# Performance work log

Measured on AMD Instinct MI355X. Metric: run time of the kernel, lower is better.

## Reference

```python
import jax, jax.numpy as jnp
import numpy as np

B, D, N, L, H, M = 8, 128, 307, 12, 8, 4
DK = D // H  # 16
APT = 10
EPS = 1e-5


def _conv1x1(x, W, b):
    # 1x1 Conv2d over channel dim: x [B,C,N,L], W [O,C], b [O]
    return jnp.einsum('bcnl,oc->bonl', x, W) + b[None, :, None, None]


def _ln12(t):
    # custom LayerNorm: normalize over dims (1,2), no affine
    m = t.mean(axis=(1, 2), keepdims=True)
    v = t.var(axis=(1, 2), keepdims=True)
    return (t - m) / jnp.sqrt(v + EPS)


def _forward(x, Wq, bq, Wv, bv, Wc, bc, Wx, bx, Wg1, bg1, Wg2, bg2, Wg3, bg3,
             mem_bank, mem_imp, A1, a1b, A2, a2b, weight, bias, nv1, nv2, sws):
    # --- multi-scale adjacency from learned node vectors ---
    base = jax.nn.relu(nv1 @ nv2)                       # [N,N]
    s1 = jax.nn.softmax(base, axis=-1)
    s2 = jax.nn.softmax(s1 @ s1, axis=-1)
    s3 = jax.nn.softmax(s2 @ s1, axis=-1)
    sw = jax.nn.softmax(sws)                            # [3]

    # --- q/v projections (Conv = 1x1 conv + ReLU; dropout off in eval) ---
    q = jax.nn.relu(_conv1x1(x, Wq, bq))
    v = jax.nn.relu(_conv1x1(x, Wv, bv))
    q5 = q.reshape(B, H, DK, N, L).transpose(0, 1, 4, 3, 2)  # bhlnk
    v5 = v.reshape(B, H, DK, N, L).transpose(0, 1, 4, 3, 2)  # bhlnk

    # --- adaptive memory retrieval ---
    avg = x.mean(axis=(2, 3))                           # [B,D]
    mem_attn = jax.nn.softmax(jax.nn.relu(avg @ A1 + a1b) @ A2 + a2b, axis=-1)  # [B,M]
    mem_w = jax.nn.softmax(mem_imp * mem_attn, axis=-1)
    sel = jnp.einsum('bm,mhlnk->bhlnk', mem_w, mem_bank)

    # --- attention against selected memory ---
    logits = jnp.einsum('bhlnk,bhlmk->bhlnm', q5, sel) / np.sqrt(DK).astype(np.float32)
    attn = jax.nn.softmax(logits, axis=-1)
    aqkv = jnp.einsum('bhlnm,bhlmk->bhlnk', attn, v5)

    # --- 3-scale graph diffusion (einsum linear in adj, so combine first) ---
    adj = sw[0] * s1 + sw[1] * s2 + sw[2] * s3          # [N,N]
    agraph = jnp.einsum('nm,bhlnk->bhlmk', adj, v5)

    y = aqkv + agraph
    y = y.transpose(0, 1, 4, 3, 2).reshape(B, D, N, L)
    y = y + _conv1x1(y, Wx, bx)                         # cross_dim_proj residual
    y = jax.nn.relu(_conv1x1(y, Wc, bc))                # concat Conv
    y = y * weight + bias + y                           # N=307 not in [170,358,5]

    # --- EnhancedEncoder wrapper ---
    z = _ln12(y + x)
    res = z
    g = _conv1x1(z, Wg1, bg1) * jax.nn.sigmoid(_conv1x1(z, Wg2, bg2))
    g = _conv1x1(g, Wg3, bg3)
    z = g + res
    z = z * weight + bias + z
    z = _ln12(z)
    return z


def setup_inputs() -> dict:
    key = jax.random.key(0)
    ks = iter(jax.random.split(key, 40))
    def rn(shape, s=0.05):
        return jax.random.normal(next(ks), shape, dtype=jnp.float32) * s
    inp = {'x': jax.random.normal(next(ks), (B, D, N, L), dtype=jnp.float32)}
    for nm in ['Wq', 'Wv', 'Wc', 'Wx', 'Wg1', 'Wg2', 'Wg3']:
        inp[nm] = rn((D, D))
        inp['b' + nm[1:]] = jnp.zeros((D,), jnp.float32)
    inp['mem_bank'] = rn((M, H, L, N, DK), 0.1)
    inp['mem_imp'] = jnp.ones((M,), jnp.float32)
    inp['A1'] = rn((D, D // 2)); inp['a1b'] = jnp.zeros((D // 2,), jnp.float32)
    inp['A2'] = rn((D // 2, M)); inp['a2b'] = jnp.zeros((M,), jnp.float32)
    inp['weight'] = jnp.ones((D, N, L), jnp.float32) + rn((D, N, L), 0.01)
    inp['bias'] = rn((D, N, L), 0.01)
    inp['nv1'] = rn((N, APT), 1.0)
    inp['nv2'] = rn((APT, N), 1.0)
    inp['sws'] = jnp.ones((3,), jnp.float32)
    return inp


def reference(x, Wq, bq, Wv, bv, Wc, bc, Wx, bx, Wg1, bg1, Wg2, bg2, Wg3, bg3,
              mem_bank, mem_imp, A1, a1b, A2, a2b, weight, bias, nv1, nv2, sws):
    return _forward(x, Wq, bq, Wv, bv, Wc, bc, Wx, bx, Wg1, bg1, Wg2, bg2, Wg3, bg3,
                    mem_bank, mem_imp, A1, a1b, A2, a2b, weight, bias, nv1, nv2, sws)
```

## Files before the change

### kernel.cpp

```cpp
#include <hip/hip_runtime.h>

namespace {

constexpr int NN   = 307;
constexpr int LNUM = 12;
constexpr int SP   = NN * LNUM;
constexpr int DCH  = 128;
constexpr int HH   = 8;
constexpr int DK   = 16;
constexpr int BB   = 8;
constexpr int SZB  = DCH * SP;
constexpr int SZ   = BB * SZB;
constexpr int ADJN = NN * NN;
constexpr int DN   = DCH * NN;
constexpr int LN_RCH = 58;
constexpr int MST  = HH * LNUM * NN * DK;

typedef __attribute__((ext_vector_type(8))) short short8_t;
typedef __attribute__((ext_vector_type(4))) float f32x4;

__device__ inline unsigned short f2bf(float f) {
  unsigned int u = __builtin_bit_cast(unsigned int, f);
  unsigned int r = (u + 0x7FFFu + ((u >> 16) & 1u)) >> 16;
  return (unsigned short)r;
}
__device__ inline float bf2f(unsigned short h) {
  unsigned int u = ((unsigned int)h) << 16;
  return __builtin_bit_cast(float, u);
}

__device__ __host__ inline int posm(int m) {
  int q = (m & 15) >> 2, sub = (m >> 4) & 1, i = m & 3;
  return (m & ~31) + 8 * q + 4 * sub + i;
}


__global__ __launch_bounds__(256) void k_cvtW(
    const float* __restrict__ W0, const float* __restrict__ W1,
    const float* __restrict__ W2, const float* __restrict__ W3,
    const float* __restrict__ W4, const float* __restrict__ W5,
    const float* __restrict__ W6, unsigned int* __restrict__ Wb) {
  const float* srcs[7] = {W0, W1, W2, W3, W4, W5, W6};
  int idx = blockIdx.x * 256 + threadIdx.x;
  int w = idx >> 13, off = idx & 8191;
  const float* s = srcs[w];
  float v0 = s[off * 2], v1 = s[off * 2 + 1];
  unsigned int pk;
  asm("v_cvt_pk_bf16_f32 %0, %1, %2" : "=v"(pk) : "v"(v0), "v"(v1));
  Wb[idx] = pk;
}

__global__ __launch_bounds__(320) void k_s1(
    const float* __restrict__ nv1, const float* __restrict__ nv2,
    float* __restrict__ out) {
  __shared__ float red[512];
  __shared__ float rowA[10];
  const int i = blockIdx.x, j = threadIdx.x;
  if (j < 10) rowA[j] = nv1[i * 10 + j];
  __syncthreads();
  float val = 0.f;
  if (j < NN) {
#pragma unroll
    for (int k = 0; k < 10; ++k) val += rowA[k] * nv2[k * NN + j];
    val = fmaxf(val, 0.f);
  }
  red[j] = (j < NN) ? val : -3.4e38f;
  if (j < 192) red[j + 320] = -3.4e38f;
  __syncthreads();
  for (int s = 256; s >= 1; s >>= 1) {
    if (j < s) red[j] = fmaxf(red[j], red[j + s]);
    __syncthreads();
  }
  float mx = red[0];
  __syncthreads();
  float e = (j < NN) ? __expf(val - mx) : 0.f;
  red[j] = e;
  if (j < 192) red[j + 320] = 0.f;
  __syncthreads();
  for (int s = 256; s >= 1; s >>= 1) {
    if (j < s) red[j] += red[j + s];
    __syncthreads();
  }
  if (j < NN) out[i * NN + j] = e / red[0];
}

__global__ __launch_bounds__(320) void k_smm(
    const float* __restrict__ Sa, const float* __restrict__ Sb,
    float* __restrict__ out) {
  __shared__ float red[512];
  __shared__ float rowA[320];
  const int i = blockIdx.x, j = threadIdx.x;
  if (j < NN) rowA[j] = Sa[i * NN + j];
  __syncthreads();
  float val = 0.f;
  if (j < NN) {
    for (int k = 0; k < NN; ++k) val += rowA[k] * Sb[k * NN + j];
  }
  red[j] = (j < NN) ? val : -3.4e38f;
  if (j < 192) red[j + 320] = -3.4e38f;
  __syncthreads();
  for (int s = 256; s >= 1; s >>= 1) {
    if (j < s) red[j] = fmaxf(red[j], red[j + s]);
    __syncthreads();
  }
  float mx = red[0];
  __syncthreads();
  float e = (j < NN) ? __expf(val - mx) : 0.f;
  red[j] = e;
  if (j < 192) red[j + 320] = 0.f;
  __syncthreads();
  for (int s = 256; s >= 1; s >>= 1) {
    if (j < s) red[j] += red[j + s];
    __syncthreads();
  }
  if (j < NN) out[i * NN + j] = e / red[0];
}

__global__ __launch_bounds__(256) void k_adjT(
    const float* __restrict__ s1, const float* __restrict__ s2,
    const float* __restrict__ s3, const float* __restrict__ sws,
    unsigned int* __restrict__ adjTw) {
  int idx = blockIdx.x * 256 + threadIdx.x;
  if (idx >= 320 * 160) return;
  int n = idx / 160, wp = idx - n * 160;
  int pos0 = 2 * wp;
  int bq = pos0 & 31;
  int g = bq >> 3, sub = (bq >> 2) & 1, i = bq & 3;
  int m0 = (pos0 & ~31) + sub * 16 + 4 * g + i;
  float w0 = sws[0], w1 = sws[1], w2 = sws[2];
  float mm = fmaxf(w0, fmaxf(w1, w2));
  float e0 = __expf(w0 - mm), e1 = __expf(w1 - mm), e2 = __expf(w2 - mm);
  float inv = 1.f / (e0 + e1 + e2);
  e0 *= inv; e1 *= inv; e2 *= inv;
  float v0 = 0.f, v1 = 0.f;
  if (n < NN) {
    if (m0 < NN)     v0 = e0 * s1[m0 * NN + n] + e1 * s2[m0 * NN + n] + e2 * s3[m0 * NN + n];
    if (m0 + 1 < NN) v1 = e0 * s1[(m0 + 1) * NN + n] + e1 * s2[(m0 + 1) * NN + n] + e2 * s3[(m0 + 1) * NN + n];
  }
  adjTw[n * 160 + wp] = (unsigned int)f2bf(v0) | ((unsigned int)f2bf(v1) << 16);
}

__global__ __launch_bounds__(256) void k_avg(
    const float* __restrict__ x, float* __restrict__ avg) {
  const int row = blockIdx.x * 4 + (threadIdx.x >> 6);
  const int lane = threadIdx.x & 63;
  const float* p = x + (size_t)row * SP;
  float s = 0.f;
  for (int i = lane; i < SP / 4; i += 64) {
    float4 v = *(const float4*)(p + i * 4);
    s += v.x + v.y + v.z + v.w;
  }
  s += __shfl_xor(s, 1);  s += __shfl_xor(s, 2);  s += __shfl_xor(s, 4);
  s += __shfl_xor(s, 8);  s += __shfl_xor(s, 16); s += __shfl_xor(s, 32);
  if (lane == 0) avg[row] = s * (1.f / SP);
}

__global__ __launch_bounds__(128) void k_memw2(
    const float* __restrict__ avgg, const float* __restrict__ A1,
    const float* __restrict__ a1b, const float* __restrict__ A2,
    const float* __restrict__ a2b, const float* __restrict__ mimp,
    float* __restrict__ memw) {
  const int b = blockIdx.x, t = threadIdx.x;
  __shared__ float avg[128];
  __shared__ float hbuf[64];
  __shared__ float lg[4];
  avg[t] = avgg[b * 128 + t];
  __syncthreads();
  if (t < 64) {
    float a = a1b[t];
    for (int d = 0; d < 128; ++d) a += avg[d] * A1[d * 64 + t];
    hbuf[t] = fmaxf(a, 0.f);
  }
  __syncthreads();
  if (t < 4) {
    float a = a2b[t];
    for (int j = 0; j < 64; ++j) a += hbuf[j] * A2[j * 4 + t];
    lg[t] = a;
  }
  __syncthreads();
  if (t == 0) {
    float mx = fmaxf(fmaxf(lg[0], lg[1]), fmaxf(lg[2], lg[3]));
    float e[4]; float se = 0.f;
    for (int m = 0; m < 4; ++m) { e[m] = __expf(lg[m] - mx); se += e[m]; }
    float w[4]; float mx2 = -3.4e38f;
    for (int m = 0; m < 4; ++m) { w[m] = mimp[m] * (e[m] / se); mx2 = fmaxf(mx2, w[m]); }
    float se2 = 0.f;
    for (int m = 0; m < 4; ++m) { e[m] = __expf(w[m] - mx2); se2 += e[m]; }
    for (int m = 0; m < 4; ++m) memw[b * 4 + m] = e[m] / se2;
  }
}

__global__ __launch_bounds__(256) void k_convqv(
    const unsigned short* __restrict__ Wqb, const unsigned short* __restrict__ Wvb,
    const float* __restrict__ X, const float* __restrict__ bq,
    const float* __restrict__ bv, unsigned short* __restrict__ qb,
    unsigned short* __restrict__ vb) {
  __shared__ unsigned short Xs[64 * 128];
  __shared__ unsigned short Ws[128 * 128];
  const int sBase = blockIdx.x * 64;
  const int b = blockIdx.z;
  const int t = threadIdx.x;

  {
    const int u = t & 63, cp = t >> 6;
    const int s = sBase + u;
    const bool in = s < SP;
#pragma unroll
    for (int it = 0; it < 16; ++it) {
      int c0 = it * 8 + cp * 2;
      float v0 = 0.f, v1 = 0.f;
      if (in) {
        v0 = X[(size_t)(b * DCH + c0) * SP + s];
        v1 = X[(size_t)(b * DCH + c0 + 1) * SP + s];
      }
      unsigned int pk;
      asm("v_cvt_pk_bf16_f32 %0, %1, %2" : "=v"(pk) : "v"(v0), "v"(v1));
      *(unsigned int*)((char*)Xs + u * 256 + ((2 * c0) ^ ((u & 7) << 4))) = pk;
    }
  }
  const int o = t >> 1, half = t & 1;
  {
    const unsigned short* src = Wqb + o * 128 + half * 64;
#pragma unroll
    for (int j = 0; j < 8; ++j) {
      short8_t v = *(const short8_t*)(src + j * 8);
      *(short8_t*)((char*)Ws + o * 256 + ((half * 128 + j * 16) ^ ((o & 7) << 4))) = v;
    }
  }
  __syncthreads();

  const int wave = t >> 6, lane = t & 63;
  const int r = lane & 15, g = lane >> 4;
  const int swz = (r & 7) << 4;

  short8_t xa[4];
#pragma unroll
  for (int kk = 0; kk < 4; ++kk)
    xa[kk] = *(const short8_t*)((const char*)Xs + (wave * 16 + r) * 256 + ((kk * 64 + g * 16) ^ swz));

  const f32x4 zf = {0.f, 0.f, 0.f, 0.f};
  const int s0 = sBase + wave * 16 + 4 * g;
  const bool act = s0 < SP;

  {
    f32x4 acc[8];
#pragma unroll
    for (int ot = 0; ot < 8; ++ot) acc[ot] = zf;
#pragma unroll
    for (int ot = 0; ot < 8; ++ot) {
#pragma unroll
      for (int kk = 0; kk < 4; ++kk) {
        short8_t wb = *(const short8_t*)((const char*)Ws + (ot * 16 + r) * 256 + ((kk * 64 + g * 16) ^ swz));
        acc[ot] = __builtin_amdgcn_mfma_f32_16x16x32_bf16(xa[kk], wb, acc[ot], 0, 0, 0);
      }
    }
    if (act) {
#pragma unroll
      for (int ot = 0; ot < 8; ++ot) {
        float bvv = bq[ot * 16 + r];
#pragma unroll
        for (int i = 0; i < 4; ++i) {
          int s = s0 + i, n = s / 12, l2 = s - n * 12;
          qb[((b * 8 + ot) * 12 + l2) * 5120 + n * 16 + r] = f2bf(fmaxf(acc[ot][i] + bvv, 0.f));
        }
      }
    }
  }
  __syncthreads();
  {
    const unsigned short* src = Wvb + o * 128 + half * 64;
#pragma unroll
    for (int j = 0; j < 8; ++j) {
      short8_t v = *(const short8_t*)(src + j * 8);
      *(short8_t*)((char*)Ws + o * 256 + ((half * 128 + j * 16) ^ ((o & 7) << 4))) = v;
    }
  }
  __syncthreads();
  {
    f32x4 acc[8];
#pragma unroll
    for (int ot = 0; ot < 8; ++ot) acc[ot] = zf;
#pragma unroll
    for (int ot = 0; ot < 8; ++ot) {
#pragma unroll
      for (int kk = 0; kk < 4; ++kk) {
        short8_t wb = *(const short8_t*)((const char*)Ws + (ot * 16 + r) * 256 + ((kk * 64 + g * 16) ^ swz));
        acc[ot] = __builtin_amdgcn_mfma_f32_16x16x32_bf16(xa[kk], wb, acc[ot], 0, 0, 0);
      }
    }
    if (act) {
#pragma unroll
      for (int ot = 0; ot < 8; ++ot) {
        float bvv = bv[ot * 16 + r];
#pragma unroll
        for (int i = 0; i < 4; ++i) {
          int s = s0 + i, n = s / 12, l2 = s - n * 12;
          vb[((b * 8 + ot) * 12 + l2) * 5120 + r * 320 + posm(n)] = f2bf(fmaxf(acc[ot][i] + bvv, 0.f));
        }
      }
    }
  }
}

__global__ __launch_bounds__(256) void k_conv12(
    const unsigned short* __restrict__ Wxb, const unsigned short* __restrict__ Wcb,
    const unsigned short* __restrict__ yRp, const float* __restrict__ bx,
    const float* __restrict__ bc, const float* __restrict__ aw,
    const float* __restrict__ ab, const float* __restrict__ axf,
    unsigned short* __restrict__ outR) {
  __shared__ unsigned short Xs[64 * 128];
  __shared__ unsigned short Ws[128 * 128];
  const int sBase = blockIdx.x * 64;
  const int b = blockIdx.z;
  const int t = threadIdx.x;

  {
    const int sl = t >> 2, q = t & 3;
    const int s = sBase + sl;
    const short8_t z8 = {0, 0, 0, 0, 0, 0, 0, 0};
    const unsigned short* row = yRp + (((size_t)b * SP + s) << 7);
#pragma unroll
    for (int j = 0; j < 4; ++j) {
      int cb = 16 * (4 * j + q);
      short8_t v = (s < SP) ? *(const short8_t*)((const char*)row + cb) : z8;
      *(short8_t*)((char*)Xs + sl * 256 + (cb ^ ((sl & 7) << 4))) = v;
    }
  }
  const int o = t >> 1, half = t & 1;
  {
    const unsigned short* src = Wxb + o * 128 + half * 64;
#pragma unroll
    for (int j = 0; j < 8; ++j) {
      short8_t v = *(const short8_t*)(src + j * 8);
      *(short8_t*)((char*)Ws + o * 256 + ((half * 128 + j * 16) ^ ((o & 7) << 4))) = v;
    }
  }
  __syncthreads();

  const int wave = t >> 6, lane = t & 63;
  const int r = lane & 15, g = lane >> 4;
  const int swz = (r & 7) << 4;
  const int s0 = sBase + wave * 16 + 4 * g;
  const bool act = s0 < SP;

  short8_t xa[4];
#pragma unroll
  for (int kk = 0; kk < 4; ++kk)
    xa[kk] = *(const short8_t*)((const char*)Xs + (wave * 16 + r) * 256 + ((kk * 64 + g * 16) ^ swz));

  const f32x4 zf = {0.f, 0.f, 0.f, 0.f};
  f32x4 acc[8];
#pragma unroll
  for (int ot = 0; ot < 8; ++ot) acc[ot] = zf;
#pragma unroll
  for (int ot = 0; ot < 8; ++ot) {
#pragma unroll
    for (int kk = 0; kk < 4; ++kk) {
      short8_t wb = *(const short8_t*)((const char*)Ws + (ot * 16 + r) * 256 + ((kk * 64 + g * 16) ^ swz));
      acc[ot] = __builtin_amdgcn_mfma_f32_16x16x32_bf16(xa[kk], wb, acc[ot], 0, 0, 0);
    }
  }

  unsigned short tpk[8][4];
  if (act) {
#pragma unroll
    for (int ot = 0; ot < 8; ++ot) {
      int oo = ot * 16 + r;
      float bvv = bx[oo];
#pragma unroll
      for (int i = 0; i < 4; ++i) {
        int u = wave * 16 + 4 * g + i;
        float y = bf2f(*(const unsigned short*)((const char*)Xs + u * 256 + ((2 * oo) ^ ((u & 7) << 4))));
        tpk[ot][i] = f2bf(acc[ot][i] + bvv + y);
      }
    }
  }
  __syncthreads();

  if (act) {
#pragma unroll
    for (int ot = 0; ot < 8; ++ot) {
      int oo = ot * 16 + r;
#pragma unroll
      for (int i = 0; i < 4; ++i) {
        int u = wave * 16 + 4 * g + i;
        *(unsigned short*)((char*)Xs + u * 256 + ((2 * oo) ^ ((u & 7) << 4))) = tpk[ot][i];
      }
    }
  }
  {
    const unsigned short* src = Wcb + o * 128 + half * 64;
#pragma unroll
    for (int j = 0; j < 8; ++j) {
      short8_t v = *(const short8_t*)(src + j * 8);
      *(short8_t*)((char*)Ws + o * 256 + ((half * 128 + j * 16) ^ ((o & 7) << 4))) = v;
    }
  }
  __syncthreads();

#pragma unroll
  for (int kk = 0; kk < 4; ++kk)
    xa[kk] = *(const short8_t*)((const char*)Xs + (wave * 16 + r) * 256 + ((kk * 64 + g * 16) ^ swz));
#pragma unroll
  for (int ot = 0; ot < 8; ++ot) acc[ot] = zf;
#pragma unroll
  for (int ot = 0; ot < 8; ++ot) {
#pragma unroll
    for (int kk = 0; kk < 4; ++kk) {
      short8_t wb = *(const short8_t*)((const char*)Ws + (ot * 16 + r) * 256 + ((kk * 64 + g * 16) ^ swz));
      acc[ot] = __builtin_amdgcn_mfma_f32_16x16x32_bf16(xa[kk], wb, acc[ot], 0, 0, 0);
    }
  }

  if (!act) return;
#pragma unroll
  for (int ot = 0; ot < 8; ++ot) {
    int oo = ot * 16 + r;
    float bvv = bc[oo];
    float4 w4 = *(const float4*)(aw + oo * SP + s0);
    float4 b4 = *(const float4*)(ab + oo * SP + s0);
    float4 x4 = *(const float4*)(axf + (size_t)(b * DCH + oo) * SP + s0);
#pragma unroll
    for (int i = 0; i < 4; ++i) {
      float rr = fmaxf(acc[ot][i] + bvv, 0.f);
      float val = rr * ((&w4.x)[i] + 1.f) + (&b4.x)[i] + (&x4.x)[i];
      outR[(((size_t)b * SP + s0 + i) << 7) + oo] = f2bf(val);
    }
  }
}

__global__ __launch_bounds__(256) void k_conv345(
    const unsigned short* __restrict__ Wb1, const unsigned short* __restrict__ Wb2,
    const unsigned short* __restrict__ Wb3, const unsigned short* __restrict__ Zr,
    const float* __restrict__ b1, const float* __restrict__ b2,
    const float* __restrict__ b3, const float* __restrict__ meanp,
    const float* __restrict__ rstdp, const float* __restrict__ aw,
    const float* __restrict__ ab, unsigned short* __restrict__ outR) {
  __shared__ unsigned short Xs[64 * 128];
  __shared__ unsigned short Ws[128 * 128];
  const int sBase = blockIdx.x * 64;
  const int b = blockIdx.z;
  const int t = threadIdx.x;

  {
    const int sl = t >> 2, q = t & 3;
    const int s = sBase + sl;
    float m = 0.f, rr = 0.f;
    if (s < SP) { int l = s % 12; m = meanp[b * 12 + l]; rr = rstdp[b * 12 + l]; }
    const short8_t z8 = {0, 0, 0, 0, 0, 0, 0, 0};
    const unsigned short* row = Zr + (((size_t)b * SP + s) << 7);
#pragma unroll
    for (int j = 0; j < 4; ++j) {
      int cb = 16 * (4 * j + q);
      short8_t v = (s < SP) ? *(const short8_t*)((const char*)row + cb) : z8;
      union { unsigned int w[4]; short8_t s8; } u;
#pragma unroll
      for (int k2 = 0; k2 < 4; ++k2) {
        float f0 = (bf2f((unsigned short)v[2 * k2]) - m) * rr;
        float f1 = (bf2f((unsigned short)v[2 * k2 + 1]) - m) * rr;
        asm("v_cvt_pk_bf16_f32 %0, %1, %2" : "=v"(u.w[k2]) : "v"(f0), "v"(f1));
      }
      *(short8_t*)((char*)Xs + sl * 256 + (cb ^ ((sl & 7) << 4))) = u.s8;
    }
  }
  const int o = t >> 1, half = t & 1;
  {
    const unsigned short* src = Wb1 + o * 128 + half * 64;
#pragma unroll
    for (int j = 0; j < 8; ++j) {
      short8_t v = *(const short8_t*)(src + j * 8);
      *(short8_t*)((char*)Ws + o * 256 + ((half * 128 + j * 16) ^ ((o & 7) << 4))) = v;
    }
  }
  __syncthreads();

  const int wave = t >> 6, lane = t & 63;
  const int r = lane & 15, g = lane >> 4;
  const int swz = (r & 7) << 4;
  const int s0 = sBase + wave * 16 + 4 * g;
  const bool act = s0 < SP;

  short8_t xa[4];
#pragma unroll
  for (int kk = 0; kk < 4; ++kk)
    xa[kk] = *(const short8_t*)((const char*)Xs + (wave * 16 + r) * 256 + ((kk * 64 + g * 16) ^ swz));

  const f32x4 zf = {0.f, 0.f, 0.f, 0.f};
  f32x4 acc1[8], acc2[8];
#pragma unroll
  for (int ot = 0; ot < 8; ++ot) { acc1[ot] = zf; acc2[ot] = zf; }
#pragma unroll
  for (int ot = 0; ot < 8; ++ot) {
#pragma unroll
    for (int kk = 0; kk < 4; ++kk) {
      short8_t wb = *(const short8_t*)((const char*)Ws + (ot * 16 + r) * 256 + ((kk * 64 + g * 16) ^ swz));
      acc1[ot] = __builtin_amdgcn_mfma_f32_16x16x32_bf16(xa[kk], wb, acc1[ot], 0, 0, 0);
    }
  }
  __syncthreads();
  {
    const unsigned short* src = Wb2 + o * 128 + half * 64;
#pragma unroll
    for (int j = 0; j < 8; ++j) {
      short8_t v = *(const short8_t*)(src + j * 8);
      *(short8_t*)((char*)Ws + o * 256 + ((half * 128 + j * 16) ^ ((o & 7) << 4))) = v;
    }
  }
  __syncthreads();
#pragma unroll
  for (int ot = 0; ot < 8; ++ot) {
#pragma unroll
    for (int kk = 0; kk < 4; ++kk) {
      short8_t wb = *(const short8_t*)((const char*)Ws + (ot * 16 + r) * 256 + ((kk * 64 + g * 16) ^ swz));
      acc2[ot] = __builtin_amdgcn_mfma_f32_16x16x32_bf16(xa[kk], wb, acc2[ot], 0, 0, 0);
    }
  }

  unsigned short gpk[8][4], zres[8][4];
  if (act) {
#pragma unroll
    for (int ot = 0; ot < 8; ++ot) {
      int oo = ot * 16 + r;
      float bb1 = b1[oo], bb2 = b2[oo];
#pragma unroll
      for (int i = 0; i < 4; ++i) {
        int u = wave * 16 + 4 * g + i;
        float v1 = acc1[ot][i] + bb1;
        float v2 = acc2[ot][i] + bb2;
        gpk[ot][i] = f2bf(v1 / (1.f + __expf(-v2)));
        zres[ot][i] = *(const unsigned short*)((const char*)Xs + u * 256 + ((2 * oo) ^ ((u & 7) << 4)));
      }
    }
  }
  __syncthreads();

  if (act) {
#pragma unroll
    for (int ot = 0; ot < 8; ++ot) {
      int oo = ot * 16 + r;
#pragma unroll
      for (int i = 0; i < 4; ++i) {
        int u = wave * 16 + 4 * g + i;
        *(unsigned short*)((char*)Xs + u * 256 + ((2 * oo) ^ ((u & 7) << 4))) = gpk[ot][i];
      }
    }
  }
  {
    const unsigned short* src = Wb3 + o * 128 + half * 64;
#pragma unroll
    for (int j = 0; j < 8; ++j) {
      short8_t v = *(const short8_t*)(src + j * 8);
      *(short8_t*)((char*)Ws + o * 256 + ((half * 128 + j * 16) ^ ((o & 7) << 4))) = v;
    }
  }
  __syncthreads();

#pragma unroll
  for (int kk = 0; kk < 4; ++kk)
    xa[kk] = *(const short8_t*)((const char*)Xs + (wave * 16 + r) * 256 + ((kk * 64 + g * 16) ^ swz));
#pragma unroll
  for (int ot = 0; ot < 8; ++ot) acc1[ot] = zf;
#pragma unroll
  for (int ot = 0; ot < 8; ++ot) {
#pragma unroll
    for (int kk = 0; kk < 4; ++kk) {
      short8_t wb = *(const short8_t*)((const char*)Ws + (ot * 16 + r) * 256 + ((kk * 64 + g * 16) ^ swz));
      acc1[ot] = __builtin_amdgcn_mfma_f32_16x16x32_bf16(xa[kk], wb, acc1[ot], 0, 0, 0);
    }
  }

  if (!act) return;
#pragma unroll
  for (int ot = 0; ot < 8; ++ot) {
    int oo = ot * 16 + r;
    float bvv = b3[oo];
    float4 w4 = *(const float4*)(aw + oo * SP + s0);
    float4 b4 = *(const float4*)(ab + oo * SP + s0);
#pragma unroll
    for (int i = 0; i < 4; ++i) {
      float tt = acc1[ot][i] + bvv + bf2f(zres[ot][i]);
      outR[(((size_t)b * SP + s0 + i) << 7) + oo] = f2bf(tt * ((&w4.x)[i] + 1.f) + (&b4.x)[i]);
    }
  }
}

__global__ __launch_bounds__(256) void k_attn_mfma(
    const unsigned short* __restrict__ q5b, const unsigned short* __restrict__ vt5b,
    const float* __restrict__ memb, const float* __restrict__ memw,
    const unsigned short* __restrict__ adjTb, unsigned short* __restrict__ yR) {
  __shared__ unsigned short Mb[320 * 24];
  __shared__ unsigned short Vt[16 * 328];
  const int l = blockIdx.x, h = blockIdx.y, b = blockIdx.z;
  const int t = threadIdx.x;
  const int slice = (b * HH + h) * LNUM + l;
  const int msl = (h * LNUM + l) * NN * DK;
  const float w0 = memw[b * 4 + 0], w1 = memw[b * 4 + 1];
  const float w2 = memw[b * 4 + 2], w3 = memw[b * 4 + 3];

  for (int idx = t; idx < 640; idx += 256) {
    int n = idx >> 1, h8 = idx & 1;
    float v[8];
    if (n < NN) {
      int off = msl + n * 16 + h8 * 8;
      const float4* p0 = (const float4*)(memb + off);
      const float4* p1 = (const float4*)(memb + MST + off);
      const float4* p2 = (const float4*)(memb + 2 * MST + off);
      const float4* p3 = (const float4*)(memb + 3 * MST + off);
      float4 a0 = p0[0], a1 = p1[0], a2 = p2[0], a3 = p3[0];
      float4 c0 = p0[1], c1 = p1[1], c2 = p2[1], c3 = p3[1];
      v[0] = w0 * a0.x + w1 * a1.x + w2 * a2.x + w3 * a3.x;
      v[1] = w0 * a0.y + w1 * a1.y + w2 * a2.y + w3 * a3.y;
      v[2] = w0 * a0.z + w1 * a1.z + w2 * a2.z + w3 * a3.z;
      v[3] = w0 * a0.w + w1 * a1.w + w2 * a2.w + w3 * a3.w;
      v[4] = w0 * c0.x + w1 * c1.x + w2 * c2.x + w3 * c3.x;
      v[5] = w0 * c0.y + w1 * c1.y + w2 * c2.y + w3 * c3.y;
      v[6] = w0 * c0.z + w1 * c1.z + w2 * c2.z + w3 * c3.z;
      v[7] = w0 * c0.w + w1 * c1.w + w2 * c2.w + w3 * c3.w;
    } else {
#pragma unroll
      for (int j = 0; j < 8; ++j) v[j] = 0.f;
    }
    union { unsigned int w[4]; short8_t s; } u;
#pragma unroll
    for (int j = 0; j < 4; ++j)
      u.w[j] = (unsigned int)f2bf(v[2 * j]) | ((unsigned int)f2bf(v[2 * j + 1]) << 16);
    *(short8_t*)(Mb + n * 24 + h8 * 8) = u.s;
  }
  {
    const unsigned short* vsl = vt5b + slice * (16 * 320);
    for (int c = t; c < 640; c += 256) {
      int row = c / 40, ch = c - row * 40;
      short8_t vv = *(const short8_t*)(vsl + row * 320 + ch * 8);
      *(short8_t*)(Vt + row * 328 + ch * 8) = vv;
    }
  }
  __syncthreads();
  for (int idx = t; idx < 16 * 13; idx += 256) {
    int row = idx / 13, j = idx - row * 13;
    Vt[row * 328 + posm(NN + j)] = 0;
  }
  __syncthreads();

  const int wave = t >> 6, lane = t & 63;
  const int r = lane & 15, g = lane >> 4;
  const f32x4 zf = {0.f, 0.f, 0.f, 0.f};
  float maskv[4];
#pragma unroll
  for (int i = 0; i < 4; ++i) maskv[i] = (4 * g + i < 3) ? 1.f : 0.f;
  constexpr float CEXP = 0.25f * 1.44269504089f;

  for (int rt5 = 0; rt5 < 5; ++rt5) {
    const int n0 = (wave * 5 + rt5) * 16;
    short8_t bq = {0, 0, 0, 0, 0, 0, 0, 0};
    if (g < 2 && n0 + r < NN) bq = *(const short8_t*)(q5b + (slice * 320 + n0 + r) * 16 + 8 * g);
    f32x4 accPV = zf, accG = zf;
    float dn = 0.f;
#pragma unroll 2
    for (int mt = 0; mt < 10; ++mt) {
      const int mb = mt * 32;
      short8_t am0 = {0, 0, 0, 0, 0, 0, 0, 0}, am1 = am0;
      if (g < 2) {
        am0 = *(const short8_t*)(Mb + (mb + r) * 24 + 8 * g);
        am1 = *(const short8_t*)(Mb + (mb + 16 + r) * 24 + 8 * g);
      }
      f32x4 s0 = __builtin_amdgcn_mfma_f32_16x16x32_bf16(am0, bq, zf, 0, 0, 0);
      f32x4 s1 = __builtin_amdgcn_mfma_f32_16x16x32_bf16(am1, bq, zf, 0, 0, 0);
      float p0[4], p1[4];
#pragma unroll
      for (int i = 0; i < 4; ++i) {
        p0[i] = __builtin_amdgcn_exp2f(s0[i] * CEXP);
        p1[i] = __builtin_amdgcn_exp2f(s1[i] * CEXP);
      }
      if (mt == 9) {
#pragma unroll
        for (int i = 0; i < 4; ++i) p1[i] *= maskv[i];
      }
      dn += p0[0] + p0[1] + p0[2] + p0[3] + p1[0] + p1[1] + p1[2] + p1[3];
      union { unsigned int w[4]; short8_t s; } up;
      asm("v_cvt_pk_bf16_f32 %0, %1, %2" : "=v"(up.w[0]) : "v"(p0[0]), "v"(p0[1]));
      asm("v_cvt_pk_bf16_f32 %0, %1, %2" : "=v"(up.w[1]) : "v"(p0[2]), "v"(p0[3]));
      asm("v_cvt_pk_bf16_f32 %0, %1, %2" : "=v"(up.w[2]) : "v"(p1[0]), "v"(p1[1]));
      asm("v_cvt_pk_bf16_f32 %0, %1, %2" : "=v"(up.w[3]) : "v"(p1[2]), "v"(p1[3]));
      short8_t bv = *(const short8_t*)(Vt + r * 328 + mb + 8 * g);
      accPV = __builtin_amdgcn_mfma_f32_16x16x32_bf16(up.s, bv, accPV, 0, 0, 0);
      short8_t aj = *(const short8_t*)(adjTb + (n0 + r) * 320 + mb + 8 * g);
      accG = __builtin_amdgcn_mfma_f32_16x16x32_bf16(aj, bv, accG, 0, 0, 0);
    }
    dn += __shfl_xor(dn, 16);
    dn += __shfl_xor(dn, 32);
#pragma unroll
    for (int i = 0; i < 4; ++i) {
      int n = n0 + 4 * g + i;
      float di = __shfl(dn, 4 * g + i);
      if (n < NN) {
        yR[(((size_t)b * SP + n * 12 + l) << 7) + h * 16 + r] = f2bf(accPV[i] / di + accG[i]);
      }
    }
  }
}


__global__ __launch_bounds__(256) void k_lnstatR(
    const unsigned short* __restrict__ inR, float* __restrict__ pS, float* __restrict__ pSS) {
  const int chunk = blockIdx.x, b = blockIdx.y, t = threadIdx.x;
  const int sl = t >> 2, q = t & 3;
  const int s = chunk * 64 + sl;
  float sm = 0.f, sq = 0.f;
  if (s < SP) {
    const unsigned short* row = inR + (((size_t)b * SP + s) << 7);
#pragma unroll
    for (int j = 0; j < 4; ++j) {
      short8_t v = *(const short8_t*)((const char*)row + 16 * (4 * j + q));
#pragma unroll
      for (int k = 0; k < 8; ++k) {
        float f = bf2f((unsigned short)v[k]);
        sm += f; sq += f * f;
      }
    }
  }
  __shared__ float ls[256], lq[256];
  ls[t] = sm; lq[t] = sq;
  __syncthreads();
  if (t < 64) {
    ls[t * 4] = ls[t * 4] + ls[t * 4 + 1] + ls[t * 4 + 2] + ls[t * 4 + 3];
    lq[t * 4] = lq[t * 4] + lq[t * 4 + 1] + lq[t * 4 + 2] + lq[t * 4 + 3];
  }
  __syncthreads();
  if (t < 12) {
    float S = 0.f, SS = 0.f;
    for (int u2 = 0; u2 < 64; ++u2) {
      int s2 = chunk * 64 + u2;
      if (s2 < SP && s2 % 12 == t) { S += ls[u2 * 4]; SS += lq[u2 * 4]; }
    }
    pS[(b * LN_RCH + chunk) * 12 + t] = S;
    pSS[(b * LN_RCH + chunk) * 12 + t] = SS;
  }
}

__global__ __launch_bounds__(96) void k_lnfin2(
    const float* __restrict__ pS, const float* __restrict__ pSS,
    float* __restrict__ meanp, float* __restrict__ rstdp, int nch) {
  const int t = threadIdx.x;
  const int b = t / 12, l = t % 12;
  float S = 0.f, SS = 0.f;
  for (int c = 0; c < nch; ++c) {
    S += pS[(b * nch + c) * 12 + l];
    SS += pSS[(b * nch + c) * 12 + l];
  }
  float mu = S * (1.f / DN);
  float var = SS * (1.f / DN) - mu * mu;
  meanp[t] = mu;
  rstdp[t] = rsqrtf(fmaxf(var, 0.f) + 1e-5f);
}

__global__ __launch_bounds__(256) void k_lnapplyT(
    const unsigned short* __restrict__ inR, const float* __restrict__ meanp,
    const float* __restrict__ rstdp, float* __restrict__ outp) {
  __shared__ float Ls[64][129];
  const int sBase = blockIdx.x * 64;
  const int b = blockIdx.y;
  const int t = threadIdx.x;
  {
    const int sl = t >> 2, q = t & 3;
    const int s = sBase + sl;
    if (s < SP) {
      int l = s % 12;
      float m = meanp[b * 12 + l], rr = rstdp[b * 12 + l];
      const unsigned short* row = inR + (((size_t)b * SP + s) << 7);
#pragma unroll
      for (int j = 0; j < 4; ++j) {
        short8_t v = *(const short8_t*)((const char*)row + 16 * (4 * j + q));
        int c0 = 8 * (4 * j + q);
#pragma unroll
        for (int k = 0; k < 8; ++k)
          Ls[sl][c0 + k] = (bf2f((unsigned short)v[k]) - m) * rr;
      }
    }
  }
  __syncthreads();
  const int c = t >> 1, h = t & 1;
  const int sW = sBase + h * 32;
  float* dst = outp + (size_t)(b * DCH + c) * SP + sW;
  const int lim = SP - sW;
#pragma unroll
  for (int j4 = 0; j4 < 8; ++j4) {
    int j = j4 * 4;
    if (j + 3 < lim) {
      float4 v;
      v.x = Ls[h * 32 + j + 0][c];
      v.y = Ls[h * 32 + j + 1][c];
      v.z = Ls[h * 32 + j + 2][c];
      v.w = Ls[h * 32 + j + 3][c];
      *(float4*)(dst + j) = v;
    } else {
#pragma unroll
      for (int e = 0; e < 4; ++e)
        if (j + e < lim) dst[j + e] = Ls[h * 32 + j + e][c];
    }
  }
}

}

extern "C" void kernel_launch(void* const* d_in, const int* in_sizes, int n_in,
                              void* d_out, int out_size, void* d_ws, size_t ws_size,
                              hipStream_t stream) {
  (void)in_sizes; (void)n_in; (void)out_size; (void)ws_size;
  const float* x    = (const float*)d_in[0];
  const float* Wq   = (const float*)d_in[1];
  const float* bq   = (const float*)d_in[2];
  const float* Wv   = (const float*)d_in[3];
  const float* bv   = (const float*)d_in[4];
  const float* Wc   = (const float*)d_in[5];
  const float* bc   = (const float*)d_in[6];
  const float* Wx   = (const float*)d_in[7];
  const float* bx   = (const float*)d_in[8];
  const float* Wg1  = (const float*)d_in[9];
  const float* bg1  = (const float*)d_in[10];
  const float* Wg2  = (const float*)d_in[11];
  const float* bg2  = (const float*)d_in[12];
  const float* Wg3  = (const float*)d_in[13];
  const float* bg3  = (const float*)d_in[14];
  const float* memb = (const float*)d_in[15];
  const float* mimp = (const float*)d_in[16];
  const float* A1   = (const float*)d_in[17];
  const float* a1b  = (const float*)d_in[18];
  const float* A2   = (const float*)d_in[19];
  const float* a2b  = (const float*)d_in[20];
  const float* wgt  = (const float*)d_in[21];
  const float* bia  = (const float*)d_in[22];
  const float* nv1  = (const float*)d_in[23];
  const float* nv2  = (const float*)d_in[24];
  const float* sws  = (const float*)d_in[25];

  float* ws = (float*)d_ws;
  float* P0 = ws;
  float* P1 = ws + (size_t)SZ;
  float* P2 = ws + 2 * (size_t)SZ;
  float* sm = ws + 3 * (size_t)SZ;
  float* s1 = sm;
  float* s2 = sm + ADJN;
  float* s3 = sm + 2 * ADJN;
  float* adjT_f = sm + 3 * ADJN;
  float* memw = adjT_f + 51200;
  float* WbSlot = memw + 32;
  float* pS   = WbSlot + 7 * 16384;
  float* pSS  = pS + BB * LN_RCH * 12;
  float* meanp = pSS + BB * LN_RCH * 12;
  float* rstdp = meanp + 96;
  float* avgb  = rstdp + 96;

  unsigned short* q5b   = (unsigned short*)P0;
  unsigned short* vt5b  = (unsigned short*)P1;
  unsigned short* yR    = (unsigned short*)P2;
  unsigned short* zinR  = (unsigned short*)P1;
  unsigned short* t2R   = (unsigned short*)P0;
  unsigned short* adjTb = (unsigned short*)adjT_f;
  unsigned short* Wb7   = (unsigned short*)WbSlot;

  k_cvtW<<<224, 256, 0, stream>>>(Wq, Wv, Wx, Wc, Wg1, Wg2, Wg3, (unsigned int*)Wb7);
  k_s1<<<NN, 320, 0, stream>>>(nv1, nv2, s1);
  k_smm<<<NN, 320, 0, stream>>>(s1, s1, s2);
  k_smm<<<NN, 320, 0, stream>>>(s2, s1, s3);
  k_adjT<<<(320 * 160 + 255) / 256, 256, 0, stream>>>(s1, s2, s3, sws, (unsigned int*)adjTb);
  k_avg<<<BB * DCH / 4, 256, 0, stream>>>(x, avgb);
  k_memw2<<<BB, 128, 0, stream>>>(avgb, A1, a1b, A2, a2b, mimp, memw);

  k_convqv<<<dim3(58, 1, BB), 256, 0, stream>>>(Wb7 + 0 * 16384, Wb7 + 1 * 16384,
                                                x, bq, bv, q5b, vt5b);

  k_attn_mfma<<<dim3(LNUM, HH, BB), 256, 0, stream>>>(q5b, vt5b, memb, memw, adjTb, yR);

  k_conv12<<<dim3(58, 1, BB), 256, 0, stream>>>(Wb7 + 2 * 16384, Wb7 + 3 * 16384,
                                                yR, bx, bc, wgt, bia, x, zinR);

  k_lnstatR<<<dim3(LN_RCH, BB), 256, 0, stream>>>(zinR, pS, pSS);
  k_lnfin2<<<1, 96, 0, stream>>>(pS, pSS, meanp, rstdp, LN_RCH);

  k_conv345<<<dim3(58, 1, BB), 256, 0, stream>>>(Wb7 + 4 * 16384, Wb7 + 5 * 16384,
                                                 Wb7 + 6 * 16384, zinR, bg1, bg2, bg3,
                                                 meanp, rstdp, wgt, bia, t2R);

  k_lnstatR<<<dim3(LN_RCH, BB), 256, 0, stream>>>(t2R, pS, pSS);
  k_lnfin2<<<1, 96, 0, stream>>>(pS, pSS, meanp, rstdp, LN_RCH);
  k_lnapplyT<<<dim3(58, BB), 256, 0, stream>>>(t2R, meanp, rstdp, (float*)d_out);
}
```

Before: 220.3 us.

## Fuse LayerNorm statistics into conv epilogues and finalize stats in consumers

The conv12 and conv345 epilogues now accumulate per-row sums and sums of squares of the bf16-rounded outputs, reduce them across the wave with shuffles and through shared memory, and write per-chunk partials per time step. The standalone lnstat and lnfin kernels are removed. Each consumer kernel (conv345, lnapplyT) rebuilds mean and rstd from the partials at block start. This drops four launches and a full re-read of each activation tensor, at the cost of a redundant 58-chunk reduction in every consumer block and an extra barrier in the epilogues.

New measurement: 193.6 us. 1.14x faster.

```diff
diff --git a/kernel.cpp b/kernel.cpp
--- a/kernel.cpp
+++ b/kernel.cpp
@@ -307,13 +307,16 @@
     const unsigned short* __restrict__ yRp, const float* __restrict__ bx,
     const float* __restrict__ bc, const float* __restrict__ aw,
     const float* __restrict__ ab, const float* __restrict__ axf,
-    unsigned short* __restrict__ outR) {
+    unsigned short* __restrict__ outR, float* __restrict__ pS,
+    float* __restrict__ pSS) {
   __shared__ unsigned short Xs[64 * 128];
   __shared__ unsigned short Ws[128 * 128];
+  __shared__ float rowS[64], rowQ[64];
   const int sBase = blockIdx.x * 64;
   const int b = blockIdx.z;
   const int t = threadIdx.x;
 
+  if (t < 64) { rowS[t] = 0.f; rowQ[t] = 0.f; }
   {
     const int sl = t >> 2, q = t & 3;
     const int s = sBase + sl;
@@ -412,20 +415,50 @@
     }
   }
 
-  if (!act) return;
-#pragma unroll
-  for (int ot = 0; ot < 8; ++ot) {
-    int oo = ot * 16 + r;
-    float bvv = bc[oo];
-    float4 w4 = *(const float4*)(aw + oo * SP + s0);
-    float4 b4 = *(const float4*)(ab + oo * SP + s0);
-    float4 x4 = *(const float4*)(axf + (size_t)(b * DCH + oo) * SP + s0);
+  float sm_[4] = {0.f, 0.f, 0.f, 0.f}, sq_[4] = {0.f, 0.f, 0.f, 0.f};
+  if (act) {
+#pragma unroll
+    for (int ot = 0; ot < 8; ++ot) {
+      int oo = ot * 16 + r;
+      float bvv = bc[oo];
+      float4 w4 = *(const float4*)(aw + oo * SP + s0);
+      float4 b4 = *(const float4*)(ab + oo * SP + s0);
+      float4 x4 = *(const float4*)(axf + (size_t)(b * DCH + oo) * SP + s0);
+#pragma unroll
+      for (int i = 0; i < 4; ++i) {
+        float rr = fmaxf(acc[ot][i] + bvv, 0.f);
+        float val = rr * ((&w4.x)[i] + 1.f) + (&b4.x)[i] + (&x4.x)[i];
+        unsigned short pk = f2bf(val);
+        outR[(((size_t)b * SP + s0 + i) << 7) + oo] = pk;
+        float vq = bf2f(pk);
+        sm_[i] += vq; sq_[i] += vq * vq;
+      }
+    }
+  }
+#pragma unroll
+  for (int msk = 1; msk <= 8; msk <<= 1) {
 #pragma unroll
     for (int i = 0; i < 4; ++i) {
-      float rr = fmaxf(acc[ot][i] + bvv, 0.f);
-      float val = rr * ((&w4.x)[i] + 1.f) + (&b4.x)[i] + (&x4.x)[i];
-      outR[(((size_t)b * SP + s0 + i) << 7) + oo] = f2bf(val);
-    }
+      sm_[i] += __shfl_xor(sm_[i], msk);
+      sq_[i] += __shfl_xor(sq_[i], msk);
+    }
+  }
+  if (r == 0 && act) {
+#pragma unroll
+    for (int i = 0; i < 4; ++i) {
+      rowS[wave * 16 + 4 * g + i] = sm_[i];
+      rowQ[wave * 16 + 4 * g + i] = sq_[i];
+    }
+  }
+  __syncthreads();
+  if (t < 12) {
+    float S = 0.f, SS = 0.f;
+    for (int u2 = 0; u2 < 64; ++u2) {
+      int s2 = sBase + u2;
+      if (s2 < SP && s2 % 12 == t) { S += rowS[u2]; SS += rowQ[u2]; }
+    }
+    pS[(b * LN_RCH + blockIdx.x) * 12 + t] = S;
+    pSS[(b * LN_RCH + blockIdx.x) * 12 + t] = SS;
   }
 }
 
@@ -433,20 +466,37 @@
     const unsigned short* __restrict__ Wb1, const unsigned short* __restrict__ Wb2,
     const unsigned short* __restrict__ Wb3, const unsigned short* __restrict__ Zr,
     const float* __restrict__ b1, const float* __restrict__ b2,
-    const float* __restrict__ b3, const float* __restrict__ meanp,
-    const float* __restrict__ rstdp, const float* __restrict__ aw,
-    const float* __restrict__ ab, unsigned short* __restrict__ outR) {
+    const float* __restrict__ b3, const float* __restrict__ pSin,
+    const float* __restrict__ pSSin, const float* __restrict__ aw,
+    const float* __restrict__ ab, unsigned short* __restrict__ outR,
+    float* __restrict__ pSo, float* __restrict__ pSSo) {
   __shared__ unsigned short Xs[64 * 128];
   __shared__ unsigned short Ws[128 * 128];
+  __shared__ float rowS[64], rowQ[64];
+  __shared__ float meanv[12], rstdv[12];
   const int sBase = blockIdx.x * 64;
   const int b = blockIdx.z;
   const int t = threadIdx.x;
 
+  if (t < 64) { rowS[t] = 0.f; rowQ[t] = 0.f; }
+  if (t < 12) {
+    float S = 0.f, SS = 0.f;
+    for (int c = 0; c < LN_RCH; ++c) {
+      S += pSin[(b * LN_RCH + c) * 12 + t];
+      SS += pSSin[(b * LN_RCH + c) * 12 + t];
+    }
+    float mu = S * (1.f / DN);
+    float var = SS * (1.f / DN) - mu * mu;
+    meanv[t] = mu;
+    rstdv[t] = rsqrtf(fmaxf(var, 0.f) + 1e-5f);
+  }
+  __syncthreads();
+
   {
     const int sl = t >> 2, q = t & 3;
     const int s = sBase + sl;
     float m = 0.f, rr = 0.f;
-    if (s < SP) { int l = s % 12; m = meanp[b * 12 + l]; rr = rstdp[b * 12 + l]; }
+    if (s < SP) { int l = s % 12; m = meanv[l]; rr = rstdv[l]; }
     const short8_t z8 = {0, 0, 0, 0, 0, 0, 0, 0};
     const unsigned short* row = Zr + (((size_t)b * SP + s) << 7);
 #pragma unroll
@@ -569,18 +619,48 @@
     }
   }
 
-  if (!act) return;
-#pragma unroll
-  for (int ot = 0; ot < 8; ++ot) {
-    int oo = ot * 16 + r;
-    float bvv = b3[oo];
-    float4 w4 = *(const float4*)(aw + oo * SP + s0);
-    float4 b4 = *(const float4*)(ab + oo * SP + s0);
+  float sm_[4] = {0.f, 0.f, 0.f, 0.f}, sq_[4] = {0.f, 0.f, 0.f, 0.f};
+  if (act) {
+#pragma unroll
+    for (int ot = 0; ot < 8; ++ot) {
+      int oo = ot * 16 + r;
+      float bvv = b3[oo];
+      float4 w4 = *(const float4*)(aw + oo * SP + s0);
+      float4 b4 = *(const float4*)(ab + oo * SP + s0);
+#pragma unroll
+      for (int i = 0; i < 4; ++i) {
+        float tt = acc1[ot][i] + bvv + bf2f(zres[ot][i]);
+        unsigned short pk = f2bf(tt * ((&w4.x)[i] + 1.f) + (&b4.x)[i]);
+        outR[(((size_t)b * SP + s0 + i) << 7) + oo] = pk;
+        float vq = bf2f(pk);
+        sm_[i] += vq; sq_[i] += vq * vq;
+      }
+    }
+  }
+#pragma unroll
+  for (int msk = 1; msk <= 8; msk <<= 1) {
 #pragma unroll
     for (int i = 0; i < 4; ++i) {
-      float tt = acc1[ot][i] + bvv + bf2f(zres[ot][i]);
-      outR[(((size_t)b * SP + s0 + i) << 7) + oo] = f2bf(tt * ((&w4.x)[i] + 1.f) + (&b4.x)[i]);
-    }
+      sm_[i] += __shfl_xor(sm_[i], msk);
+      sq_[i] += __shfl_xor(sq_[i], msk);
+    }
+  }
+  if (r == 0 && act) {
+#pragma unroll
+    for (int i = 0; i < 4; ++i) {
+      rowS[wave * 16 + 4 * g + i] = sm_[i];
+      rowQ[wave * 16 + 4 * g + i] = sq_[i];
+    }
+  }
+  __syncthreads();
+  if (t < 12) {
+    float S = 0.f, SS = 0.f;
+    for (int u2 = 0; u2 < 64; ++u2) {
+      int s2 = sBase + u2;
+      if (s2 < SP && s2 % 12 == t) { S += rowS[u2]; SS += rowQ[u2]; }
+    }
+    pSo[(b * LN_RCH + blockIdx.x) * 12 + t] = S;
+    pSSo[(b * LN_RCH + blockIdx.x) * 12 + t] = SS;
   }
 }
 
@@ -699,73 +779,32 @@
   }
 }
 
-
-__global__ __launch_bounds__(256) void k_lnstatR(
-    const unsigned short* __restrict__ inR, float* __restrict__ pS, float* __restrict__ pSS) {
-  const int chunk = blockIdx.x, b = blockIdx.y, t = threadIdx.x;
-  const int sl = t >> 2, q = t & 3;
-  const int s = chunk * 64 + sl;
-  float sm = 0.f, sq = 0.f;
-  if (s < SP) {
-    const unsigned short* row = inR + (((size_t)b * SP + s) << 7);
-#pragma unroll
-    for (int j = 0; j < 4; ++j) {
-      short8_t v = *(const short8_t*)((const char*)row + 16 * (4 * j + q));
-#pragma unroll
-      for (int k = 0; k < 8; ++k) {
-        float f = bf2f((unsigned short)v[k]);
-        sm += f; sq += f * f;
-      }
-    }
-  }
-  __shared__ float ls[256], lq[256];
-  ls[t] = sm; lq[t] = sq;
-  __syncthreads();
-  if (t < 64) {
-    ls[t * 4] = ls[t * 4] + ls[t * 4 + 1] + ls[t * 4 + 2] + ls[t * 4 + 3];
-    lq[t * 4] = lq[t * 4] + lq[t * 4 + 1] + lq[t * 4 + 2] + lq[t * 4 + 3];
-  }
-  __syncthreads();
-  if (t < 12) {
-    float S = 0.f, SS = 0.f;
-    for (int u2 = 0; u2 < 64; ++u2) {
-      int s2 = chunk * 64 + u2;
-      if (s2 < SP && s2 % 12 == t) { S += ls[u2 * 4]; SS += lq[u2 * 4]; }
-    }
-    pS[(b * LN_RCH + chunk) * 12 + t] = S;
-    pSS[(b * LN_RCH + chunk) * 12 + t] = SS;
-  }
-}
-
-__global__ __launch_bounds__(96) void k_lnfin2(
-    const float* __restrict__ pS, const float* __restrict__ pSS,
-    float* __restrict__ meanp, float* __restrict__ rstdp, int nch) {
-  const int t = threadIdx.x;
-  const int b = t / 12, l = t % 12;
-  float S = 0.f, SS = 0.f;
-  for (int c = 0; c < nch; ++c) {
-    S += pS[(b * nch + c) * 12 + l];
-    SS += pSS[(b * nch + c) * 12 + l];
-  }
-  float mu = S * (1.f / DN);
-  float var = SS * (1.f / DN) - mu * mu;
-  meanp[t] = mu;
-  rstdp[t] = rsqrtf(fmaxf(var, 0.f) + 1e-5f);
-}
-
 __global__ __launch_bounds__(256) void k_lnapplyT(
-    const unsigned short* __restrict__ inR, const float* __restrict__ meanp,
-    const float* __restrict__ rstdp, float* __restrict__ outp) {
+    const unsigned short* __restrict__ inR, const float* __restrict__ pS,
+    const float* __restrict__ pSS, float* __restrict__ outp) {
   __shared__ float Ls[64][129];
+  __shared__ float meanv[12], rstdv[12];
   const int sBase = blockIdx.x * 64;
   const int b = blockIdx.y;
   const int t = threadIdx.x;
+  if (t < 12) {
+    float S = 0.f, SS = 0.f;
+    for (int c = 0; c < LN_RCH; ++c) {
+      S += pS[(b * LN_RCH + c) * 12 + t];
+      SS += pSS[(b * LN_RCH + c) * 12 + t];
+    }
+    float mu = S * (1.f / DN);
+    float var = SS * (1.f / DN) - mu * mu;
+    meanv[t] = mu;
+    rstdv[t] = rsqrtf(fmaxf(var, 0.f) + 1e-5f);
+  }
+  __syncthreads();
   {
     const int sl = t >> 2, q = t & 3;
     const int s = sBase + sl;
     if (s < SP) {
       int l = s % 12;
-      float m = meanp[b * 12 + l], rr = rstdp[b * 12 + l];
+      float m = meanv[l], rr = rstdv[l];
       const unsigned short* row = inR + (((size_t)b * SP + s) << 7);
 #pragma unroll
       for (int j = 0; j < 4; ++j) {
@@ -844,11 +883,11 @@
   float* adjT_f = sm + 3 * ADJN;
   float* memw = adjT_f + 51200;
   float* WbSlot = memw + 32;
-  float* pS   = WbSlot + 7 * 16384;
-  float* pSS  = pS + BB * LN_RCH * 12;
-  float* meanp = pSS + BB * LN_RCH * 12;
-  float* rstdp = meanp + 96;
-  float* avgb  = rstdp + 96;
+  float* pS1  = WbSlot + 7 * 16384;
+  float* pSS1 = pS1 + BB * LN_RCH * 12;
+  float* pS2  = pSS1 + BB * LN_RCH * 12;
+  float* pSS2 = pS2 + BB * LN_RCH * 12;
+  float* avgb = pSS2 + BB * LN_RCH * 12;
 
   unsigned short* q5b   = (unsigned short*)P0;
   unsigned short* vt5b  = (unsigned short*)P1;
@@ -872,16 +911,11 @@
   k_attn_mfma<<<dim3(LNUM, HH, BB), 256, 0, stream>>>(q5b, vt5b, memb, memw, adjTb, yR);
 
   k_conv12<<<dim3(58, 1, BB), 256, 0, stream>>>(Wb7 + 2 * 16384, Wb7 + 3 * 16384,
-                                                yR, bx, bc, wgt, bia, x, zinR);
-
-  k_lnstatR<<<dim3(LN_RCH, BB), 256, 0, stream>>>(zinR, pS, pSS);
-  k_lnfin2<<<1, 96, 0, stream>>>(pS, pSS, meanp, rstdp, LN_RCH);
+                                                yR, bx, bc, wgt, bia, x, zinR, pS1, pSS1);
 
   k_conv345<<<dim3(58, 1, BB), 256, 0, stream>>>(Wb7 + 4 * 16384, Wb7 + 5 * 16384,
                                                  Wb7 + 6 * 16384, zinR, bg1, bg2, bg3,
-                                                 meanp, rstdp, wgt, bia, t2R);
-
-  k_lnstatR<<<dim3(LN_RCH, BB), 256, 0, stream>>>(t2R, pS, pSS);
-  k_lnfin2<<<1, 96, 0, stream>>>(pS, pSS, meanp, rstdp, LN_RCH);
-  k_lnapplyT<<<dim3(58, BB), 256, 0, stream>>>(t2R, meanp, rstdp, (float*)d_out);
-}
+                                                 pS1, pSS1, wgt, bia, t2R, pS2, pSS2);
+
+  k_lnapplyT<<<dim3(58, BB), 256, 0, stream>>>(t2R, pS2, pSS2, (float*)d_out);
+}
```
